# Kernel tuning notes

Hardware: AMD Instinct MI355X
Metric: run time of the kernel (lower is better)

Reference implementation:

```python
import jax, jax.numpy as jnp
import numpy as np

B, T, H = 16384, 64, 64
REG = 300
T10_LO, T10_HI = 0.2, 5.0
M0_LO, M0_HI = 0.1, 20.0


def setup_inputs() -> dict:
    key = jax.random.key(0)
    ks = jax.random.split(key, 40)
    std = 1.0 / np.sqrt(H)
    u = lambda k, shape: jax.random.uniform(k, shape, jnp.float32, -std, std)
    inp = {
        "X_fa": jax.random.normal(ks[0], (B, T), jnp.float32),
        "X_last": jax.random.normal(ks[1], (B, T), jnp.float32),
        "X_mean": jax.random.normal(ks[2], (B, T), jnp.float32),
        "X_mask": (jax.random.uniform(ks[3], (B, T)) < 0.7).astype(jnp.float32),
        "X_delta": jax.random.uniform(ks[4], (B, T), jnp.float32, 0.0, 2.0),
        "fa_vals": jax.random.uniform(ks[5], (B, T), jnp.float32, 0.05, 0.6),
        "TR_vals": jax.random.uniform(ks[6], (B, 1), jnp.float32, 0.003, 0.01),
        # GRU-D cell params (torch Linear convention: y = x @ W.T + b)
        "W_gx": u(ks[7], (1, 1)), "b_gx": u(ks[8], (1,)),
        "W_gh": u(ks[9], (H, 1)), "b_gh": u(ks[10], (H,)),
        "W_xc": u(ks[11], (3 * H, 1)), "b_xc": u(ks[12], (3 * H,)),
        "W_hn": u(ks[13], (H, H)),
        "W_hc": u(ks[14], (2 * H, H)),
        "W_mc": u(ks[15], (3 * H, 1)),
        # attention scores
        "W_sT": u(ks[16], (1, H)), "W_sM": u(ks[17], (1, H)),
        # reg_T10 MLP
        "Wt1": u(ks[18], (REG, H)), "bt1": u(ks[19], (REG,)),
        "Wt2": u(ks[20], (REG, REG)), "bt2": u(ks[21], (REG,)),
        "Wt3": u(ks[22], (1, REG)), "bt3": u(ks[23], (1,)),
        # reg_M0 MLP
        "Wm1": u(ks[24], (REG, H)), "bm1": u(ks[25], (REG,)),
        "Wm2": u(ks[26], (REG, REG)), "bm2": u(ks[27], (REG,)),
        "Wm3": u(ks[28], (1, REG)), "bm3": u(ks[29], (1,)),
    }
    return inp


def _forward(X_fa, X_last, X_mean, X_mask, X_delta, fa_vals, TR_vals,
             W_gx, b_gx, W_gh, b_gh, W_xc, b_xc, W_hn, W_hc, W_mc,
             W_sT, W_sM, Wt1, bt1, Wt2, bt2, Wt3, bt3, Wm1, bm1, Wm2, bm2, Wm3, bm3):
    Bv = X_fa.shape[0]
    Hd = W_gh.shape[0]
    tb = lambda a: a.T[:, :, None]  # [B,T] -> [T,B,1]
    xs = (tb(X_fa), tb(X_mask), tb(X_delta), tb(X_last), tb(X_mean))
    h0 = jnp.zeros((Bv, Hd), X_fa.dtype)

    def step(h, x):
        xi, m, d, xl, xm = x  # each [B,1]
        gx = jnp.exp(-jax.nn.relu(d @ W_gx.T + b_gx))            # [B,1]
        X = m * xi + (1 - m) * gx * xl + (1 - m) * (1 - gx) * xm  # [B,1]
        gh = jnp.exp(-jax.nn.relu(d @ W_gh.T + b_gh))            # [B,H]
        h = gh * h
        x_z, x_r, x_n = jnp.split(X @ W_xc.T + b_xc, 3, axis=1)
        h_z, h_r = jnp.split(h @ W_hc.T, 2, axis=1)
        m_z, m_r, m_n = jnp.split(m @ W_mc.T, 3, axis=1)
        z = jax.nn.sigmoid(x_z + h_z + m_z)
        r = jax.nn.sigmoid(x_r + h_r + m_r)
        h_til = jnp.tanh(x_n + (r * h) @ W_hn.T + m_n)
        h = (1 - z) * h + z * h_til
        return h, (h, X[:, 0])

    _, (out_tbh, Xg_tb) = jax.lax.scan(step, h0, xs)
    out = jnp.transpose(out_tbh, (1, 0, 2))  # [B,T,H]
    X_gru = Xg_tb.T                           # [B,T]

    sT = jax.nn.softmax(out @ W_sT.T, axis=1)  # [B,T,1], softmax over time
    sM = jax.nn.softmax(out @ W_sM.T, axis=1)
    hid_T = jnp.sum(out * sT, axis=1)  # [B,H]
    hid_M = jnp.sum(out * sM, axis=1)

    def reg(h, W1, b1, W2, b2, W3, b3):
        h = jax.nn.elu(h @ W1.T + b1)
        h = jax.nn.elu(h @ W2.T + b2)
        return h @ W3.T + b3  # [B,1]

    t_raw = reg(hid_T, Wt1, bt1, Wt2, bt2, Wt3, bt3)
    m_raw = reg(hid_M, Wm1, bm1, Wm2, bm2, Wm3, bm3)
    T10 = T10_LO + jax.nn.sigmoid(t_raw) * (T10_HI - T10_LO)  # [B,1]
    M0 = M0_LO + jax.nn.sigmoid(m_raw) * (M0_HI - M0_LO)      # [B,1]

    R1 = 1.0 / T10                       # [B,1]
    e = jnp.exp(-TR_vals * R1)           # [B,1]
    X_out = (1 - e) * jnp.sin(fa_vals) / (1 - jnp.cos(fa_vals) * e)  # [B,T]
    X_out = X_out * M0
    return X_out, T10, M0, out, X_gru


def reference(X_fa, X_last, X_mean, X_mask, X_delta, fa_vals, TR_vals,
              W_gx, b_gx, W_gh, b_gh, W_xc, b_xc, W_hn, W_hc, W_mc,
              W_sT, W_sM, Wt1, bt1, Wt2, bt2, Wt3, bt3, Wm1, bm1, Wm2, bm2, Wm3, bm3):
    return _forward(X_fa, X_last, X_mean, X_mask, X_delta, fa_vals, TR_vals,
                    W_gx, b_gx, W_gh, b_gh, W_xc, b_xc, W_hn, W_hc, W_mc,
                    W_sT, W_sM, Wt1, bt1, Wt2, bt2, Wt3, bt3, Wm1, bm1, Wm2, bm2, Wm3, bm3)
```

## Files before the change

### kernel.cpp

```cpp
#include <hip/hip_runtime.h>

#define B_N 16384
#define T_N 64
#define H_N 64
#define XOUT_OFF 0
#define T10_OFF  (B_N * T_N)
#define M0_OFF   (T10_OFF + B_N)
#define OUT_OFF  (M0_OFF + B_N)
#define XGRU_OFF (OUT_OFF + B_N * T_N * H_N)

#define WS_HIDT 0
#define WS_HIDM (WS_HIDT + B_N * 64 * 4)
#define WS_W1T_HI (WS_HIDM + B_N * 64 * 4)
#define WS_W1T_LO (WS_W1T_HI + 304 * 64 * 2)
#define WS_W1M_HI (WS_W1T_LO + 304 * 64 * 2)
#define WS_W1M_LO (WS_W1M_HI + 304 * 64 * 2)
#define WS_W2T_HI (WS_W1M_LO + 304 * 64 * 2)
#define WS_W2T_LO (WS_W2T_HI + 304 * 320 * 2)
#define WS_W2M_HI (WS_W2T_LO + 304 * 320 * 2)
#define WS_W2M_LO (WS_W2M_HI + 304 * 320 * 2)

typedef float  f32x4  __attribute__((ext_vector_type(4)));
typedef __bf16 bf16x8 __attribute__((ext_vector_type(8)));
typedef __bf16 bf16x4 __attribute__((ext_vector_type(4)));

__device__ __forceinline__ f32x4 mfma16(bf16x8 a, bf16x8 b, f32x4 c) {
  return __builtin_amdgcn_mfma_f32_16x16x32_bf16(a, b, c, 0, 0, 0);
}
__device__ __forceinline__ void split8v(const float* v, bf16x8& hi, bf16x8& lo) {
#pragma unroll
  for (int i = 0; i < 8; ++i) {
    __bf16 h = (__bf16)v[i];
    hi[i] = h;
    lo[i] = (__bf16)(v[i] - (float)h);
  }
}
__device__ __forceinline__ void split4v(const float* v, bf16x4& hi, bf16x4& lo) {
#pragma unroll
  for (int i = 0; i < 4; ++i) {
    __bf16 h = (__bf16)v[i];
    hi[i] = h;
    lo[i] = (__bf16)(v[i] - (float)h);
  }
}
__device__ __forceinline__ float sigm(float x) { return 1.f / (1.f + __expf(-x)); }
__device__ __forceinline__ float tanh_f(float x) { return 1.f - 2.f / (__expf(2.f * x) + 1.f); }

__global__ __launch_bounds__(256, 1) void k_gru(
    const float* __restrict__ Xfa, const float* __restrict__ Xlast,
    const float* __restrict__ Xmean, const float* __restrict__ Xmask,
    const float* __restrict__ Xdelta,
    const float* __restrict__ Wgx, const float* __restrict__ bgx,
    const float* __restrict__ Wgh, const float* __restrict__ bgh,
    const float* __restrict__ Wxc, const float* __restrict__ bxc,
    const float* __restrict__ Whn, const float* __restrict__ Whc,
    const float* __restrict__ Wmc,
    const float* __restrict__ WsT, const float* __restrict__ WsM,
    float* __restrict__ dout, float* __restrict__ hidT, float* __restrict__ hidM) {
  __shared__ __align__(16) unsigned char smem[43776];
  const int tid = threadIdx.x;
  const int wv = tid >> 6, l = tid & 63, b16 = l & 15, g4 = l >> 4;
  const int b = blockIdx.x * 64 + wv * 16 + b16;

  {
    float* cf = (float*)(smem + 24576);
    for (int i = tid; i < 704; i += 256) {
      float v;
      if (i < 64) v = Wgh[i];
      else if (i < 128) v = bgh[i - 64];
      else if (i < 320) v = Wxc[i - 128];
      else if (i < 512) v = Wmc[i - 320];
      else v = bxc[i - 512];
      cf[i] = v;
    }
  }
  bf16x8 whc_lo[8][2], whn_lo[4][2];
#pragma unroll
  for (int jt = 0; jt < 8; ++jt) {
#pragma unroll
    for (int kt = 0; kt < 2; ++kt) {
      const int row = jt * 16 + b16;
      const float* src = Whc + row * 64 + kt * 32 + g4 * 8;
      float v[8];
      *(float4*)&v[0] = *(const float4*)src;
      *(float4*)&v[4] = *(const float4*)(src + 4);
      bf16x8 hi, lo;
      split8v(v, hi, lo);
      whc_lo[jt][kt] = lo;
      *(bf16x8*)(smem + row * 128 + ((kt * 64 + g4 * 16) ^ ((row & 7) << 4))) = hi;
    }
  }
#pragma unroll
  for (int jt = 0; jt < 4; ++jt) {
#pragma unroll
    for (int kt = 0; kt < 2; ++kt) {
      const int row = jt * 16 + b16;
      const float* src = Whn + row * 64 + kt * 32 + g4 * 8;
      float v[8];
      *(float4*)&v[0] = *(const float4*)src;
      *(float4*)&v[4] = *(const float4*)(src + 4);
      bf16x8 hi, lo;
      split8v(v, hi, lo);
      whn_lo[jt][kt] = lo;
      *(bf16x8*)(smem + 16384 + row * 128 + ((kt * 64 + g4 * 16) ^ ((row & 7) << 4))) = hi;
    }
  }
  __syncthreads();

  const float* cWgh = (const float*)(smem + 24576);
  const float* cBgh = cWgh + 64;
  const float* cWxc = cWgh + 128;
  const float* cWmc = cWgh + 320;
  const float* cBxc = cWgh + 512;

  float wsTv[4][4], wsMv[4][4];
#pragma unroll
  for (int jt = 0; jt < 4; ++jt)
#pragma unroll
    for (int i = 0; i < 4; ++i) {
      const int j = jt * 16 + g4 * 4 + i;
      wsTv[jt][i] = WsT[j];
      wsMv[jt][i] = WsM[j];
    }

  float h[4][4] = {};
  float aT[4][4] = {}, aM[4][4] = {};
  float mT = -1e30f, lT = 0.f, mM = -1e30f, lM = 0.f;
  const float wgx0 = Wgx[0], bgx0 = bgx[0];

  const int ib = b * T_N;
  float p_xi = Xfa[ib], p_mm = Xmask[ib], p_dd = Xdelta[ib], p_xl = Xlast[ib], p_xm = Xmean[ib];
  const int hoff = 27392 + wv * 4096;
  float* outp = dout + OUT_OFF;

  for (int t = 0; t < T_N; ++t) {
    const float xi = p_xi, mm = p_mm, dd = p_dd, xl = p_xl, xm = p_xm;
    const int tn = (t + 1 < T_N) ? t + 1 : T_N - 1;
    p_xi = Xfa[ib + tn]; p_mm = Xmask[ib + tn]; p_dd = Xdelta[ib + tn];
    p_xl = Xlast[ib + tn]; p_xm = Xmean[ib + tn];

    const float gx = __expf(-fmaxf(0.f, dd * wgx0 + bgx0));
    const float X = mm * xi + (1.f - mm) * gx * xl + (1.f - mm) * (1.f - gx) * xm;
    if (l < 16) dout[XGRU_OFF + ib + t] = X;

#pragma unroll
    for (int jt = 0; jt < 4; ++jt) {
      const int j0 = jt * 16 + g4 * 4;
      f32x4 wg = *(const f32x4*)(cWgh + j0);
      f32x4 bg = *(const f32x4*)(cBgh + j0);
      float v[4];
#pragma unroll
      for (int i = 0; i < 4; ++i) {
        const float ghv = __expf(-fmaxf(0.f, dd * wg[i] + bg[i]));
        h[jt][i] *= ghv;
        v[i] = h[jt][i];
      }
      bf16x4 hi4, lo4;
      split4v(v, hi4, lo4);
      const int off = (jt * 32 + g4 * 8) ^ ((b16 & 7) << 4);
      *(bf16x4*)(smem + hoff + b16 * 128 + off) = hi4;
      *(bf16x4*)(smem + hoff + 2048 + b16 * 128 + off) = lo4;
    }
    bf16x8 bh[2], bl[2];
#pragma unroll
    for (int kt = 0; kt < 2; ++kt) {
      const int off = (kt * 64 + g4 * 16) ^ ((b16 & 7) << 4);
      bh[kt] = *(const bf16x8*)(smem + hoff + b16 * 128 + off);
      bl[kt] = *(const bf16x8*)(smem + hoff + 2048 + b16 * 128 + off);
    }
    f32x4 accZ[4], accR[4];
#pragma unroll
    for (int jt = 0; jt < 8; ++jt) {
      f32x4 acc = {0.f, 0.f, 0.f, 0.f};
#pragma unroll
      for (int kt = 0; kt < 2; ++kt) {
        const int row = jt * 16 + b16;
        bf16x8 ahi = *(const bf16x8*)(smem + row * 128 + ((kt * 64 + g4 * 16) ^ ((row & 7) << 4)));
        acc = mfma16(ahi, bh[kt], acc);
        acc = mfma16(whc_lo[jt][kt], bh[kt], acc);
        acc = mfma16(ahi, bl[kt], acc);
      }
      if (jt < 4) accZ[jt] = acc; else accR[jt - 4] = acc;
    }
    float zz[4][4];
#pragma unroll
    for (int jt = 0; jt < 4; ++jt) {
      const int j0 = jt * 16 + g4 * 4;
      f32x4 cwz = *(const f32x4*)(cWxc + j0);
      f32x4 cbz = *(const f32x4*)(cBxc + j0);
      f32x4 cmz = *(const f32x4*)(cWmc + j0);
      f32x4 cwr = *(const f32x4*)(cWxc + 64 + j0);
      f32x4 cbr = *(const f32x4*)(cBxc + 64 + j0);
      f32x4 cmr = *(const f32x4*)(cWmc + 64 + j0);
      float v[4];
#pragma unroll
      for (int i = 0; i < 4; ++i) {
        const float z = sigm(accZ[jt][i] + X * cwz[i] + cbz[i] + mm * cmz[i]);
        const float r = sigm(accR[jt][i] + X * cwr[i] + cbr[i] + mm * cmr[i]);
        zz[jt][i] = z;
        v[i] = r * h[jt][i];
      }
      bf16x4 hi4, lo4;
      split4v(v, hi4, lo4);
      const int off = (jt * 32 + g4 * 8) ^ ((b16 & 7) << 4);
      *(bf16x4*)(smem + hoff + b16 * 128 + off) = hi4;
      *(bf16x4*)(smem + hoff + 2048 + b16 * 128 + off) = lo4;
    }
    bf16x8 ch[2], cl[2];
#pragma unroll
    for (int kt = 0; kt < 2; ++kt) {
      const int off = (kt * 64 + g4 * 16) ^ ((b16 & 7) << 4);
      ch[kt] = *(const bf16x8*)(smem + hoff + b16 * 128 + off);
      cl[kt] = *(const bf16x8*)(smem + hoff + 2048 + b16 * 128 + off);
    }
    f32x4 accN[4];
#pragma unroll
    for (int jt = 0; jt < 4; ++jt) {
      f32x4 acc = {0.f, 0.f, 0.f, 0.f};
#pragma unroll
      for (int kt = 0; kt < 2; ++kt) {
        const int row = jt * 16 + b16;
        bf16x8 ahi =
            *(const bf16x8*)(smem + 16384 + row * 128 + ((kt * 64 + g4 * 16) ^ ((row & 7) << 4)));
        acc = mfma16(ahi, ch[kt], acc);
        acc = mfma16(whn_lo[jt][kt], ch[kt], acc);
        acc = mfma16(ahi, cl[kt], acc);
      }
      accN[jt] = acc;
    }
    float scT = 0.f, scM = 0.f;
#pragma unroll
    for (int jt = 0; jt < 4; ++jt) {
      const int j0 = jt * 16 + g4 * 4;
      f32x4 cwn = *(const f32x4*)(cWxc + 128 + j0);
      f32x4 cbn = *(const f32x4*)(cBxc + 128 + j0);
      f32x4 cmn = *(const f32x4*)(cWmc + 128 + j0);
      f32x4 ho;
#pragma unroll
      for (int i = 0; i < 4; ++i) {
        const float pre = accN[jt][i] + X * cwn[i] + cbn[i] + mm * cmn[i];
        const float ht = tanh_f(pre);
        const float hn = (1.f - zz[jt][i]) * h[jt][i] + zz[jt][i] * ht;
        h[jt][i] = hn;
        ho[i] = hn;
        scT += hn * wsTv[jt][i];
        scM += hn * wsMv[jt][i];
      }
      *(f32x4*)(outp + (ib + t) * 64 + j0) = ho;
    }
    scT += __shfl_xor(scT, 16); scT += __shfl_xor(scT, 32);
    scM += __shfl_xor(scM, 16); scM += __shfl_xor(scM, 32);
    {
      const float mn = fmaxf(mT, scT);
      const float s = __expf(mT - mn), p = __expf(scT - mn);
      lT = lT * s + p;
#pragma unroll
      for (int jt = 0; jt < 4; ++jt)
#pragma unroll
        for (int i = 0; i < 4; ++i) aT[jt][i] = aT[jt][i] * s + p * h[jt][i];
      mT = mn;
    }
    {
      const float mn = fmaxf(mM, scM);
      const float s = __expf(mM - mn), p = __expf(scM - mn);
      lM = lM * s + p;
#pragma unroll
      for (int jt = 0; jt < 4; ++jt)
#pragma unroll
        for (int i = 0; i < 4; ++i) aM[jt][i] = aM[jt][i] * s + p * h[jt][i];
      mM = mn;
    }
  }
  const float invT = 1.f / lT, invM = 1.f / lM;
#pragma unroll
  for (int jt = 0; jt < 4; ++jt) {
    const int j0 = jt * 16 + g4 * 4;
    f32x4 vT, vM;
#pragma unroll
    for (int i = 0; i < 4; ++i) { vT[i] = aT[jt][i] * invT; vM[i] = aM[jt][i] * invM; }
    *(f32x4*)(hidT + b * 64 + j0) = vT;
    *(f32x4*)(hidM + b * 64 + j0) = vM;
  }
}

__device__ __forceinline__ void wsplit(float v, unsigned short* hi, unsigned short* lo, int idx) {
  union { __bf16 b; unsigned short u; } c;
  __bf16 hb = (__bf16)v;
  c.b = hb; hi[idx] = c.u;
  c.b = (__bf16)(v - (float)hb); lo[idx] = c.u;
}
__global__ void k_prep(const float* __restrict__ Wt1, const float* __restrict__ Wm1,
                       const float* __restrict__ Wt2, const float* __restrict__ Wm2,
                       unsigned short* w1t_hi, unsigned short* w1t_lo,
                       unsigned short* w1m_hi, unsigned short* w1m_lo,
                       unsigned short* w2t_hi, unsigned short* w2t_lo,
                       unsigned short* w2m_hi, unsigned short* w2m_lo) {
  const int i = blockIdx.x * 256 + threadIdx.x;
  if (i < 304 * 64) {
    const int r = i >> 6, c = i & 63;
    const float vt = (r < 300) ? Wt1[r * 64 + c] : 0.f;
    const float vm = (r < 300) ? Wm1[r * 64 + c] : 0.f;
    wsplit(vt, w1t_hi, w1t_lo, i);
    wsplit(vm, w1m_hi, w1m_lo, i);
  }
  {
    const int r = i / 320, c = i - r * 320;
    const bool ok = (r < 300) && (c < 300);
    const float vt = ok ? Wt2[r * 300 + c] : 0.f;
    const float vm = ok ? Wm2[r * 300 + c] : 0.f;
    wsplit(vt, w2t_hi, w2t_lo, i);
    wsplit(vm, w2m_hi, w2m_lo, i);
  }
}

__global__ __launch_bounds__(256, 2) void k_mlp(
    const float* __restrict__ hidT, const float* __restrict__ hidM,
    const unsigned short* __restrict__ w1t_hi, const unsigned short* __restrict__ w1t_lo,
    const unsigned short* __restrict__ w1m_hi, const unsigned short* __restrict__ w1m_lo,
    const unsigned short* __restrict__ w2t_hi, const unsigned short* __restrict__ w2t_lo,
    const unsigned short* __restrict__ w2m_hi, const unsigned short* __restrict__ w2m_lo,
    const float* __restrict__ bt1, const float* __restrict__ bt2,
    const float* __restrict__ Wt3, const float* __restrict__ bt3,
    const float* __restrict__ bm1, const float* __restrict__ bm2,
    const float* __restrict__ Wm3, const float* __restrict__ bm3,
    float* __restrict__ dout) {
  __shared__ __align__(16) unsigned char smem[44608];
  const int tid = threadIdx.x;
  const int blk = blockIdx.x & 255;
  const bool isM = blockIdx.x >= 256;
  const float* hid = isM ? hidM : hidT;
  const unsigned short* w1hi = isM ? w1m_hi : w1t_hi;
  const unsigned short* w1lo = isM ? w1m_lo : w1t_lo;
  const unsigned short* w2hi = isM ? w2m_hi : w2t_hi;
  const unsigned short* w2lo = isM ? w2m_lo : w2t_lo;
  const float* b1 = isM ? bm1 : bt1;
  const float* b2 = isM ? bm2 : bt2;
  const float* w3 = isM ? Wm3 : Wt3;
  const float b3 = (isM ? bm3 : bt3)[0];
  const float LOV = isM ? 0.1f : 0.2f;
  const float HIV = isM ? 20.f : 5.0f;
  float* headp = dout + (isM ? M0_OFF : T10_OFF);

  float* sb1 = (float*)(smem + 40960);
  float* sb2 = (float*)(smem + 42176);
  float* sw3 = (float*)(smem + 43392);
  for (int i = tid; i < 304; i += 256) {
    sb1[i] = (i < 300) ? b1[i] : 0.f;
    sb2[i] = (i < 300) ? b2[i] : 0.f;
    sw3[i] = (i < 300) ? w3[i] : 0.f;
  }
  __syncthreads();

  const int wv = tid >> 6, l = tid & 63, b16 = l & 15, g4 = l >> 4;
  const int b = blk * 64 + wv * 16 + b16;
  const int h1off = wv * 10240;

  bf16x8 b1h[2], b1l[2];
#pragma unroll
  for (int kt = 0; kt < 2; ++kt) {
    const float* hp = hid + b * 64 + kt * 32 + g4 * 8;
    float v[8];
    *(float4*)&v[0] = *(const float4*)hp;
    *(float4*)&v[4] = *(const float4*)(hp + 4);
    split8v(v, b1h[kt], b1l[kt]);
  }
  f32x4 acc1[19];
#pragma unroll
  for (int jt = 0; jt < 19; ++jt) {
    f32x4 acc = {0.f, 0.f, 0.f, 0.f};
#pragma unroll
    for (int kt = 0; kt < 2; ++kt) {
      const int row = jt * 16 + b16;
      bf16x8 ahi = *(const bf16x8*)(w1hi + row * 64 + kt * 32 + g4 * 8);
      bf16x8 alo = *(const bf16x8*)(w1lo + row * 64 + kt * 32 + g4 * 8);
      acc = mfma16(ahi, b1h[kt], acc);
      acc = mfma16(alo, b1h[kt], acc);
      acc = mfma16(ahi, b1l[kt], acc);
    }
    acc1[jt] = acc;
  }
  if (g4 == 0) {
#pragma unroll
    for (int q = 0; q < 4; ++q) {
      const int off = (608 + q * 8) ^ ((b16 & 7) << 4);
      *(unsigned long long*)(smem + h1off + b16 * 640 + off) = 0ull;
    }
  }
#pragma unroll
  for (int jt = 0; jt < 19; ++jt) {
    bf16x4 hv;
#pragma unroll
    for (int i = 0; i < 4; ++i) {
      const int j = jt * 16 + g4 * 4 + i;
      const float v = acc1[jt][i] + sb1[j];
      const float e = (v > 0.f) ? v : (__expf(v) - 1.f);
      hv[i] = (__bf16)e;
    }
    const int off = (jt * 32 + g4 * 8) ^ ((b16 & 7) << 4);
    *(bf16x4*)(smem + h1off + b16 * 640 + off) = hv;
  }
  bf16x8 bh2[10];
#pragma unroll
  for (int kt = 0; kt < 10; ++kt) {
    const int off = (kt * 64 + g4 * 16) ^ ((b16 & 7) << 4);
    bh2[kt] = *(const bf16x8*)(smem + h1off + b16 * 640 + off);
  }
  float raw = 0.f;
#pragma unroll
  for (int jt = 0; jt < 19; ++jt) {
    f32x4 acc = {0.f, 0.f, 0.f, 0.f};
#pragma unroll
    for (int kt = 0; kt < 10; ++kt) {
      const int row = jt * 16 + b16;
      bf16x8 ahi = *(const bf16x8*)(w2hi + row * 320 + kt * 32 + g4 * 8);
      bf16x8 alo = *(const bf16x8*)(w2lo + row * 320 + kt * 32 + g4 * 8);
      acc = mfma16(ahi, bh2[kt], acc);
      acc = mfma16(alo, bh2[kt], acc);
    }
#pragma unroll
    for (int i = 0; i < 4; ++i) {
      const int j = jt * 16 + g4 * 4 + i;
      const float v = acc[i] + sb2[j];
      const float e = (v > 0.f) ? v : (__expf(v) - 1.f);
      raw += e * sw3[j];
    }
  }
  raw += __shfl_xor(raw, 16);
  raw += __shfl_xor(raw, 32);
  if (l < 16) {
    const float rr = raw + b3;
    headp[b] = LOV + (HIV - LOV) / (1.f + __expf(-rr));
  }
}

__global__ void k_final(const float* __restrict__ fav, const float* __restrict__ TR,
                        float* __restrict__ dout) {
  const int i = blockIdx.x * 256 + threadIdx.x;
  const int bb = i >> 6;
  const float T10v = dout[T10_OFF + bb];
  const float M0v = dout[M0_OFF + bb];
  const float e = __expf(-TR[bb] / T10v);
  const float fa = fav[i];
  float s, c;
  __sincosf(fa, &s, &c);
  dout[i] = (1.f - e) * s / (1.f - c * e) * M0v;
}

extern "C" void kernel_launch(void* const* d_in, const int* in_sizes, int n_in,
                              void* d_out, int out_size, void* d_ws, size_t ws_size,
                              hipStream_t stream) {
  const float* Xfa   = (const float*)d_in[0];
  const float* Xlast = (const float*)d_in[1];
  const float* Xmean = (const float*)d_in[2];
  const float* Xmask = (const float*)d_in[3];
  const float* Xdelta= (const float*)d_in[4];
  const float* fav   = (const float*)d_in[5];
  const float* TR    = (const float*)d_in[6];
  const float* Wgx   = (const float*)d_in[7];
  const float* bgx   = (const float*)d_in[8];
  const float* Wgh   = (const float*)d_in[9];
  const float* bgh   = (const float*)d_in[10];
  const float* Wxc   = (const float*)d_in[11];
  const float* bxc   = (const float*)d_in[12];
  const float* Whn   = (const float*)d_in[13];
  const float* Whc   = (const float*)d_in[14];
  const float* Wmc   = (const float*)d_in[15];
  const float* WsT   = (const float*)d_in[16];
  const float* WsM   = (const float*)d_in[17];
  const float* Wt1   = (const float*)d_in[18];
  const float* bt1   = (const float*)d_in[19];
  const float* Wt2   = (const float*)d_in[20];
  const float* bt2   = (const float*)d_in[21];
  const float* Wt3   = (const float*)d_in[22];
  const float* bt3   = (const float*)d_in[23];
  const float* Wm1   = (const float*)d_in[24];
  const float* bm1   = (const float*)d_in[25];
  const float* Wm2   = (const float*)d_in[26];
  const float* bm2   = (const float*)d_in[27];
  const float* Wm3   = (const float*)d_in[28];
  const float* bm3   = (const float*)d_in[29];

  float* dout = (float*)d_out;
  char* ws = (char*)d_ws;
  float* hidT = (float*)(ws + WS_HIDT);
  float* hidM = (float*)(ws + WS_HIDM);
  unsigned short* w1t_hi = (unsigned short*)(ws + WS_W1T_HI);
  unsigned short* w1t_lo = (unsigned short*)(ws + WS_W1T_LO);
  unsigned short* w1m_hi = (unsigned short*)(ws + WS_W1M_HI);
  unsigned short* w1m_lo = (unsigned short*)(ws + WS_W1M_LO);
  unsigned short* w2t_hi = (unsigned short*)(ws + WS_W2T_HI);
  unsigned short* w2t_lo = (unsigned short*)(ws + WS_W2T_LO);
  unsigned short* w2m_hi = (unsigned short*)(ws + WS_W2M_HI);
  unsigned short* w2m_lo = (unsigned short*)(ws + WS_W2M_LO);

  k_prep<<<380, 256, 0, stream>>>(Wt1, Wm1, Wt2, Wm2, w1t_hi, w1t_lo, w1m_hi, w1m_lo,
                                  w2t_hi, w2t_lo, w2m_hi, w2m_lo);
  k_gru<<<256, 256, 0, stream>>>(Xfa, Xlast, Xmean, Xmask, Xdelta, Wgx, bgx, Wgh, bgh, Wxc, bxc,
                                 Whn, Whc, Wmc, WsT, WsM, dout, hidT, hidM);
  k_mlp<<<512, 256, 0, stream>>>(hidT, hidM, w1t_hi, w1t_lo, w1m_hi, w1m_lo, w2t_hi, w2t_lo,
                                 w2m_hi, w2m_lo, bt1, bt2, Wt3, bt3, bm1, bm2, Wm3, bm3, dout);
  k_final<<<4096, 256, 0, stream>>>(fav, TR, dout);
}
```

Before: 684.7 us.

## Split GRU hidden dimension across waves with shared-state exchange per timestep

Restructures the GRU kernel so each block handles 16 batch rows. Its four waves each own a 16-column slice of the hidden state instead of each wave owning all 64 columns for its own rows. The hi/lo weight fragments are now held in registers and shared memory per wave. The input and mask contributions and the biases are folded into one extra MFMA by packing them into an extended bf16 vector. The online softmax drops its running max and accumulates raw exponentials of the scores, which are shared through LDS. This quadruples the grid, lowers register and LDS use to allow more blocks per CU, and swaps divides for reciprocal approximations, at the cost of two block barriers per timestep and no overflow protection in the attention softmax.

```diff
diff --git a/kernel.cpp b/kernel.cpp
--- a/kernel.cpp
+++ b/kernel.cpp
@@ -43,10 +43,14 @@
     lo[i] = (__bf16)(v[i] - (float)h);
   }
 }
-__device__ __forceinline__ float sigm(float x) { return 1.f / (1.f + __expf(-x)); }
-__device__ __forceinline__ float tanh_f(float x) { return 1.f - 2.f / (__expf(2.f * x) + 1.f); }
-
-__global__ __launch_bounds__(256, 1) void k_gru(
+__device__ __forceinline__ float sigm(float x) {
+  return __builtin_amdgcn_rcpf(1.f + __expf(-x));
+}
+__device__ __forceinline__ float tanh_f(float x) {
+  return 1.f - 2.f * __builtin_amdgcn_rcpf(__expf(2.f * x) + 1.f);
+}
+
+__global__ __launch_bounds__(256, 4) void k_gru(
     const float* __restrict__ Xfa, const float* __restrict__ Xlast,
     const float* __restrict__ Xmean, const float* __restrict__ Xmask,
     const float* __restrict__ Xdelta,
@@ -57,80 +61,75 @@
     const float* __restrict__ Wmc,
     const float* __restrict__ WsT, const float* __restrict__ WsM,
     float* __restrict__ dout, float* __restrict__ hidT, float* __restrict__ hidM) {
-  __shared__ __align__(16) unsigned char smem[43776];
+  __shared__ __align__(16) unsigned char smem[33280];
   const int tid = threadIdx.x;
   const int wv = tid >> 6, l = tid & 63, b16 = l & 15, g4 = l >> 4;
-  const int b = blockIdx.x * 64 + wv * 16 + b16;
-
-  {
-    float* cf = (float*)(smem + 24576);
-    for (int i = tid; i < 704; i += 256) {
-      float v;
-      if (i < 64) v = Wgh[i];
-      else if (i < 128) v = bgh[i - 64];
-      else if (i < 320) v = Wxc[i - 128];
-      else if (i < 512) v = Wmc[i - 320];
-      else v = bxc[i - 512];
-      cf[i] = v;
-    }
-  }
-  bf16x8 whc_lo[8][2], whn_lo[4][2];
-#pragma unroll
-  for (int jt = 0; jt < 8; ++jt) {
-#pragma unroll
-    for (int kt = 0; kt < 2; ++kt) {
-      const int row = jt * 16 + b16;
-      const float* src = Whc + row * 64 + kt * 32 + g4 * 8;
-      float v[8];
-      *(float4*)&v[0] = *(const float4*)src;
-      *(float4*)&v[4] = *(const float4*)(src + 4);
-      bf16x8 hi, lo;
-      split8v(v, hi, lo);
-      whc_lo[jt][kt] = lo;
-      *(bf16x8*)(smem + row * 128 + ((kt * 64 + g4 * 16) ^ ((row & 7) << 4))) = hi;
-    }
-  }
-#pragma unroll
-  for (int jt = 0; jt < 4; ++jt) {
-#pragma unroll
-    for (int kt = 0; kt < 2; ++kt) {
-      const int row = jt * 16 + b16;
-      const float* src = Whn + row * 64 + kt * 32 + g4 * 8;
-      float v[8];
-      *(float4*)&v[0] = *(const float4*)src;
-      *(float4*)&v[4] = *(const float4*)(src + 4);
-      bf16x8 hi, lo;
-      split8v(v, hi, lo);
-      whn_lo[jt][kt] = lo;
-      *(bf16x8*)(smem + 16384 + row * 128 + ((kt * 64 + g4 * 16) ^ ((row & 7) << 4))) = hi;
-    }
-  }
+  const int brow = blockIdx.x * 16 + b16;
+
+  for (int c = tid; c < 1536; c += 256) {
+    const float* src;
+    int row, kc, base;
+    if (c < 1024) { row = c >> 3; kc = c & 7; src = Whc + row * 64 + kc * 8; base = 0; }
+    else { int c2 = c - 1024; row = c2 >> 3; kc = c2 & 7; src = Whn + row * 64 + kc * 8; base = 16384; }
+    float v[8];
+    *(float4*)&v[0] = *(const float4*)src;
+    *(float4*)&v[4] = *(const float4*)(src + 4);
+    bf16x8 hi, lo;
+    split8v(v, hi, lo);
+    *(bf16x8*)(smem + base + row * 128 + ((kc * 16) ^ ((row & 7) << 4))) = lo;
+  }
+
+  const int zrow = wv * 16 + b16;
+  const int rrow = 64 + wv * 16 + b16;
+  const int nrow = wv * 16 + b16;
+  bf16x8 wz_hi[2], wr_hi[2], wn_hi[2];
+#pragma unroll
+  for (int kt = 0; kt < 2; ++kt) {
+    float v[8];
+    bf16x8 hi, lo;
+    const float* s1 = Whc + zrow * 64 + kt * 32 + g4 * 8;
+    *(float4*)&v[0] = *(const float4*)s1; *(float4*)&v[4] = *(const float4*)(s1 + 4);
+    split8v(v, hi, lo); wz_hi[kt] = hi;
+    const float* s2 = Whc + rrow * 64 + kt * 32 + g4 * 8;
+    *(float4*)&v[0] = *(const float4*)s2; *(float4*)&v[4] = *(const float4*)(s2 + 4);
+    split8v(v, hi, lo); wr_hi[kt] = hi;
+    const float* s3 = Whn + nrow * 64 + kt * 32 + g4 * 8;
+    *(float4*)&v[0] = *(const float4*)s3; *(float4*)&v[4] = *(const float4*)(s3 + 4);
+    split8v(v, hi, lo); wn_hi[kt] = hi;
+  }
+  bf16x8 ez = {}, er = {}, en = {};
+  if (g4 == 0) {
+    const int jz = zrow, jr = rrow, jn = 128 + nrow;
+    float Wv, Mv, bv;
+    __bf16 wh, mh, bh;
+#define MKEXT(dst, WIDX, MIDX, BIDX)                                   \
+    Wv = Wxc[WIDX]; Mv = Wmc[MIDX]; bv = bxc[BIDX];                    \
+    wh = (__bf16)Wv; mh = (__bf16)Mv; bh = (__bf16)bv;                 \
+    dst[0] = wh; dst[1] = (__bf16)(Wv - (float)wh); dst[2] = wh;       \
+    dst[3] = mh; dst[4] = (__bf16)(Mv - (float)mh);                    \
+    dst[5] = bh; dst[6] = (__bf16)(bv - (float)bh); dst[7] = (__bf16)0.f;
+    MKEXT(ez, jz, jz, jz)
+    MKEXT(er, jr, jr, jr)
+    MKEXT(en, jn, jn, jn)
+#undef MKEXT
+  }
+  float wgh4[4], bgh4[4], wsT4[4], wsM4[4];
+#pragma unroll
+  for (int i = 0; i < 4; ++i) {
+    const int j = wv * 16 + g4 * 4 + i;
+    wgh4[i] = Wgh[j]; bgh4[i] = bgh[j];
+    wsT4[i] = WsT[j]; wsM4[i] = WsM[j];
+  }
+  const float wgx0 = Wgx[0], bgx0 = bgx[0];
+
   __syncthreads();
 
-  const float* cWgh = (const float*)(smem + 24576);
-  const float* cBgh = cWgh + 64;
-  const float* cWxc = cWgh + 128;
-  const float* cWmc = cWgh + 320;
-  const float* cBxc = cWgh + 512;
-
-  float wsTv[4][4], wsMv[4][4];
-#pragma unroll
-  for (int jt = 0; jt < 4; ++jt)
-#pragma unroll
-    for (int i = 0; i < 4; ++i) {
-      const int j = jt * 16 + g4 * 4 + i;
-      wsTv[jt][i] = WsT[j];
-      wsMv[jt][i] = WsM[j];
-    }
-
-  float h[4][4] = {};
-  float aT[4][4] = {}, aM[4][4] = {};
-  float mT = -1e30f, lT = 0.f, mM = -1e30f, lM = 0.f;
-  const float wgx0 = Wgx[0], bgx0 = bgx[0];
-
-  const int ib = b * T_N;
+  float hcur[4] = {}, aT[4] = {}, aM[4] = {};
+  float lT = 0.f, lM = 0.f;
+
+  const int ib = brow * T_N;
   float p_xi = Xfa[ib], p_mm = Xmask[ib], p_dd = Xdelta[ib], p_xl = Xlast[ib], p_xm = Xmean[ib];
-  const int hoff = 27392 + wv * 4096;
+  const int swz = (b16 & 7) << 4;
   float* outp = dout + OUT_OFF;
 
   for (int t = 0; t < T_N; ++t) {
@@ -139,148 +138,127 @@
     p_xi = Xfa[ib + tn]; p_mm = Xmask[ib + tn]; p_dd = Xdelta[ib + tn];
     p_xl = Xlast[ib + tn]; p_xm = Xmean[ib + tn];
 
-    const float gx = __expf(-fmaxf(0.f, dd * wgx0 + bgx0));
-    const float X = mm * xi + (1.f - mm) * gx * xl + (1.f - mm) * (1.f - gx) * xm;
-    if (l < 16) dout[XGRU_OFF + ib + t] = X;
-
-#pragma unroll
-    for (int jt = 0; jt < 4; ++jt) {
-      const int j0 = jt * 16 + g4 * 4;
-      f32x4 wg = *(const f32x4*)(cWgh + j0);
-      f32x4 bg = *(const f32x4*)(cBgh + j0);
+    float hd[4];
+    {
       float v[4];
 #pragma unroll
       for (int i = 0; i < 4; ++i) {
-        const float ghv = __expf(-fmaxf(0.f, dd * wg[i] + bg[i]));
-        h[jt][i] *= ghv;
-        v[i] = h[jt][i];
+        const float gh = __expf(-fmaxf(0.f, dd * wgh4[i] + bgh4[i]));
+        hd[i] = hcur[i] * gh;
+        v[i] = hd[i];
       }
       bf16x4 hi4, lo4;
       split4v(v, hi4, lo4);
-      const int off = (jt * 32 + g4 * 8) ^ ((b16 & 7) << 4);
-      *(bf16x4*)(smem + hoff + b16 * 128 + off) = hi4;
-      *(bf16x4*)(smem + hoff + 2048 + b16 * 128 + off) = lo4;
-    }
-    bf16x8 bh[2], bl[2];
+      const int off = (wv * 32 + g4 * 8) ^ swz;
+      *(bf16x4*)(smem + 24576 + b16 * 128 + off) = hi4;
+      *(bf16x4*)(smem + 26624 + b16 * 128 + off) = lo4;
+    }
+    const float gx = __expf(-fmaxf(0.f, dd * wgx0 + bgx0));
+    const float X = mm * xi + (1.f - mm) * gx * xl + (1.f - mm) * (1.f - gx) * xm;
+    if (wv == 0 && g4 == 0) dout[XGRU_OFF + ib + t] = X;
+    bf16x8 bext = {};
+    if (g4 == 0) {
+      const __bf16 xh = (__bf16)X;
+      bext[0] = xh; bext[1] = xh; bext[2] = (__bf16)(X - (float)xh);
+      const __bf16 mb = (__bf16)mm;
+      bext[3] = mb; bext[4] = mb;
+      bext[5] = (__bf16)1.f; bext[6] = (__bf16)1.f; bext[7] = (__bf16)0.f;
+    }
+    __syncthreads();
+
+    if (t > 0) {
+      const f32x4 a = *(const f32x4*)(smem + 32768 + b16 * 32);
+      const f32x4 c = *(const f32x4*)(smem + 32768 + b16 * 32 + 16);
+      const float pT = __expf(a[0] + a[2] + c[0] + c[2]);
+      const float pM = __expf(a[1] + a[3] + c[1] + c[3]);
+      lT += pT; lM += pM;
+#pragma unroll
+      for (int i = 0; i < 4; ++i) { aT[i] += pT * hcur[i]; aM[i] += pM * hcur[i]; }
+    }
+
+    f32x4 accZ = {0.f, 0.f, 0.f, 0.f}, accR = {0.f, 0.f, 0.f, 0.f};
 #pragma unroll
     for (int kt = 0; kt < 2; ++kt) {
-      const int off = (kt * 64 + g4 * 16) ^ ((b16 & 7) << 4);
-      bh[kt] = *(const bf16x8*)(smem + hoff + b16 * 128 + off);
-      bl[kt] = *(const bf16x8*)(smem + hoff + 2048 + b16 * 128 + off);
-    }
-    f32x4 accZ[4], accR[4];
-#pragma unroll
-    for (int jt = 0; jt < 8; ++jt) {
-      f32x4 acc = {0.f, 0.f, 0.f, 0.f};
-#pragma unroll
-      for (int kt = 0; kt < 2; ++kt) {
-        const int row = jt * 16 + b16;
-        bf16x8 ahi = *(const bf16x8*)(smem + row * 128 + ((kt * 64 + g4 * 16) ^ ((row & 7) << 4)));
-        acc = mfma16(ahi, bh[kt], acc);
-        acc = mfma16(whc_lo[jt][kt], bh[kt], acc);
-        acc = mfma16(ahi, bl[kt], acc);
-      }
-      if (jt < 4) accZ[jt] = acc; else accR[jt - 4] = acc;
-    }
-    float zz[4][4];
-#pragma unroll
-    for (int jt = 0; jt < 4; ++jt) {
-      const int j0 = jt * 16 + g4 * 4;
-      f32x4 cwz = *(const f32x4*)(cWxc + j0);
-      f32x4 cbz = *(const f32x4*)(cBxc + j0);
-      f32x4 cmz = *(const f32x4*)(cWmc + j0);
-      f32x4 cwr = *(const f32x4*)(cWxc + 64 + j0);
-      f32x4 cbr = *(const f32x4*)(cBxc + 64 + j0);
-      f32x4 cmr = *(const f32x4*)(cWmc + 64 + j0);
-      float v[4];
-#pragma unroll
-      for (int i = 0; i < 4; ++i) {
-        const float z = sigm(accZ[jt][i] + X * cwz[i] + cbz[i] + mm * cmz[i]);
-        const float r = sigm(accR[jt][i] + X * cwr[i] + cbr[i] + mm * cmr[i]);
-        zz[jt][i] = z;
-        v[i] = r * h[jt][i];
-      }
+      const int boff = (kt * 64 + g4 * 16) ^ swz;
+      const bf16x8 bh = *(const bf16x8*)(smem + 24576 + b16 * 128 + boff);
+      const bf16x8 bl = *(const bf16x8*)(smem + 26624 + b16 * 128 + boff);
+      const int aoff = (kt * 64 + g4 * 16);
+      const bf16x8 zlo = *(const bf16x8*)(smem + zrow * 128 + (aoff ^ ((zrow & 7) << 4)));
+      const bf16x8 rlo = *(const bf16x8*)(smem + rrow * 128 + (aoff ^ ((rrow & 7) << 4)));
+      accZ = mfma16(wz_hi[kt], bh, accZ);
+      accZ = mfma16(zlo, bh, accZ);
+      accZ = mfma16(wz_hi[kt], bl, accZ);
+      accR = mfma16(wr_hi[kt], bh, accR);
+      accR = mfma16(rlo, bh, accR);
+      accR = mfma16(wr_hi[kt], bl, accR);
+    }
+    accZ = mfma16(ez, bext, accZ);
+    accR = mfma16(er, bext, accR);
+
+    float zz[4], rh[4];
+#pragma unroll
+    for (int i = 0; i < 4; ++i) {
+      zz[i] = sigm(accZ[i]);
+      rh[i] = sigm(accR[i]) * hd[i];
+    }
+    {
       bf16x4 hi4, lo4;
-      split4v(v, hi4, lo4);
-      const int off = (jt * 32 + g4 * 8) ^ ((b16 & 7) << 4);
-      *(bf16x4*)(smem + hoff + b16 * 128 + off) = hi4;
-      *(bf16x4*)(smem + hoff + 2048 + b16 * 128 + off) = lo4;
-    }
-    bf16x8 ch[2], cl[2];
+      split4v(rh, hi4, lo4);
+      const int off = (wv * 32 + g4 * 8) ^ swz;
+      *(bf16x4*)(smem + 28672 + b16 * 128 + off) = hi4;
+      *(bf16x4*)(smem + 30720 + b16 * 128 + off) = lo4;
+    }
+    __syncthreads();
+
+    f32x4 accN = {0.f, 0.f, 0.f, 0.f};
 #pragma unroll
     for (int kt = 0; kt < 2; ++kt) {
-      const int off = (kt * 64 + g4 * 16) ^ ((b16 & 7) << 4);
-      ch[kt] = *(const bf16x8*)(smem + hoff + b16 * 128 + off);
-      cl[kt] = *(const bf16x8*)(smem + hoff + 2048 + b16 * 128 + off);
-    }
-    f32x4 accN[4];
-#pragma unroll
-    for (int jt = 0; jt < 4; ++jt) {
-      f32x4 acc = {0.f, 0.f, 0.f, 0.f};
-#pragma unroll
-      for (int kt = 0; kt < 2; ++kt) {
-        const int row = jt * 16 + b16;
-        bf16x8 ahi =
-            *(const bf16x8*)(smem + 16384 + row * 128 + ((kt * 64 + g4 * 16) ^ ((row & 7) << 4)));
-        acc = mfma16(ahi, ch[kt], acc);
-        acc = mfma16(whn_lo[jt][kt], ch[kt], acc);
-        acc = mfma16(ahi, cl[kt], acc);
-      }
-      accN[jt] = acc;
-    }
+      const int boff = (kt * 64 + g4 * 16) ^ swz;
+      const bf16x8 ch = *(const bf16x8*)(smem + 28672 + b16 * 128 + boff);
+      const bf16x8 cl = *(const bf16x8*)(smem + 30720 + b16 * 128 + boff);
+      const bf16x8 nlo =
+          *(const bf16x8*)(smem + 16384 + nrow * 128 + ((kt * 64 + g4 * 16) ^ ((nrow & 7) << 4)));
+      accN = mfma16(wn_hi[kt], ch, accN);
+      accN = mfma16(nlo, ch, accN);
+      accN = mfma16(wn_hi[kt], cl, accN);
+    }
+    accN = mfma16(en, bext, accN);
+
+    f32x4 ho;
     float scT = 0.f, scM = 0.f;
 #pragma unroll
-    for (int jt = 0; jt < 4; ++jt) {
-      const int j0 = jt * 16 + g4 * 4;
-      f32x4 cwn = *(const f32x4*)(cWxc + 128 + j0);
-      f32x4 cbn = *(const f32x4*)(cBxc + 128 + j0);
-      f32x4 cmn = *(const f32x4*)(cWmc + 128 + j0);
-      f32x4 ho;
-#pragma unroll
-      for (int i = 0; i < 4; ++i) {
-        const float pre = accN[jt][i] + X * cwn[i] + cbn[i] + mm * cmn[i];
-        const float ht = tanh_f(pre);
-        const float hn = (1.f - zz[jt][i]) * h[jt][i] + zz[jt][i] * ht;
-        h[jt][i] = hn;
-        ho[i] = hn;
-        scT += hn * wsTv[jt][i];
-        scM += hn * wsMv[jt][i];
-      }
-      *(f32x4*)(outp + (ib + t) * 64 + j0) = ho;
-    }
+    for (int i = 0; i < 4; ++i) {
+      const float ht = tanh_f(accN[i]);
+      const float hn = (1.f - zz[i]) * hd[i] + zz[i] * ht;
+      hcur[i] = hn;
+      ho[i] = hn;
+      scT += hn * wsT4[i];
+      scM += hn * wsM4[i];
+    }
+    *(f32x4*)(outp + (ib + t) * 64 + wv * 16 + g4 * 4) = ho;
     scT += __shfl_xor(scT, 16); scT += __shfl_xor(scT, 32);
     scM += __shfl_xor(scM, 16); scM += __shfl_xor(scM, 32);
-    {
-      const float mn = fmaxf(mT, scT);
-      const float s = __expf(mT - mn), p = __expf(scT - mn);
-      lT = lT * s + p;
-#pragma unroll
-      for (int jt = 0; jt < 4; ++jt)
-#pragma unroll
-        for (int i = 0; i < 4; ++i) aT[jt][i] = aT[jt][i] * s + p * h[jt][i];
-      mT = mn;
-    }
-    {
-      const float mn = fmaxf(mM, scM);
-      const float s = __expf(mM - mn), p = __expf(scM - mn);
-      lM = lM * s + p;
-#pragma unroll
-      for (int jt = 0; jt < 4; ++jt)
-#pragma unroll
-        for (int i = 0; i < 4; ++i) aM[jt][i] = aM[jt][i] * s + p * h[jt][i];
-      mM = mn;
-    }
+    if (l < 16) {
+      float2 sc = {scT, scM};
+      *(float2*)(smem + 32768 + b16 * 32 + wv * 8) = sc;
+    }
+  }
+  __syncthreads();
+  {
+    const f32x4 a = *(const f32x4*)(smem + 32768 + b16 * 32);
+    const f32x4 c = *(const f32x4*)(smem + 32768 + b16 * 32 + 16);
+    const float pT = __expf(a[0] + a[2] + c[0] + c[2]);
+    const float pM = __expf(a[1] + a[3] + c[1] + c[3]);
+    lT += pT; lM += pM;
+#pragma unroll
+    for (int i = 0; i < 4; ++i) { aT[i] += pT * hcur[i]; aM[i] += pM * hcur[i]; }
   }
   const float invT = 1.f / lT, invM = 1.f / lM;
-#pragma unroll
-  for (int jt = 0; jt < 4; ++jt) {
-    const int j0 = jt * 16 + g4 * 4;
-    f32x4 vT, vM;
-#pragma unroll
-    for (int i = 0; i < 4; ++i) { vT[i] = aT[jt][i] * invT; vM[i] = aM[jt][i] * invM; }
-    *(f32x4*)(hidT + b * 64 + j0) = vT;
-    *(f32x4*)(hidM + b * 64 + j0) = vM;
-  }
+  f32x4 vT, vM;
+#pragma unroll
+  for (int i = 0; i < 4; ++i) { vT[i] = aT[i] * invT; vM[i] = aM[i] * invM; }
+  *(f32x4*)(hidT + brow * 64 + wv * 16 + g4 * 4) = vT;
+  *(f32x4*)(hidM + brow * 64 + wv * 16 + g4 * 4) = vM;
 }
 
 __device__ __forceinline__ void wsplit(float v, unsigned short* hi, unsigned short* lo, int idx) {
@@ -495,8 +473,8 @@
 
   k_prep<<<380, 256, 0, stream>>>(Wt1, Wm1, Wt2, Wm2, w1t_hi, w1t_lo, w1m_hi, w1m_lo,
                                   w2t_hi, w2t_lo, w2m_hi, w2m_lo);
-  k_gru<<<256, 256, 0, stream>>>(Xfa, Xlast, Xmean, Xmask, Xdelta, Wgx, bgx, Wgh, bgh, Wxc, bxc,
-                                 Whn, Whc, Wmc, WsT, WsM, dout, hidT, hidM);
+  k_gru<<<1024, 256, 0, stream>>>(Xfa, Xlast, Xmean, Xmask, Xdelta, Wgx, bgx, Wgh, bgh, Wxc, bxc,
+                                  Whn, Whc, Wmc, WsT, WsM, dout, hidT, hidM);
   k_mlp<<<512, 256, 0, stream>>>(hidT, hidM, w1t_hi, w1t_lo, w1m_hi, w1m_lo, w2t_hi, w2t_lo,
                                  w2m_hi, w2m_lo, bt1, bt2, Wt3, bt3, bm1, bm2, Wm3, bm3, dout);
   k_final<<<4096, 256, 0, stream>>>(fav, TR, dout);
```

Measured after the change: 697.0 us. No clear change (+1.8%).
